# Kernel tuning notes

Measured on AMD Instinct MI355X. Metric: run time of the kernel, lower is better.

The kernel has to match this reference:

```python
import jax, jax.numpy as jnp
import numpy as np

B = 4
T, Hh, Ww = 16, 32, 32
C = 256
HEADS = 8
WIN = 4
SHIFT = 2
MLP = 1024


def _rel_pos_index(w):
    coords = np.stack(np.meshgrid(np.arange(w), np.arange(w), np.arange(w), indexing='ij')).reshape(3, -1)
    rc = (coords[:, :, None] - coords[:, None, :]).transpose(1, 2, 0)
    rc[:, :, 0] += w - 1
    rc[:, :, 1] += w - 1
    rc[:, :, 2] += w - 1
    rc[:, :, 0] *= (2 * w - 1) * (2 * w - 1)
    rc[:, :, 1] *= 2 * w - 1
    return rc.sum(-1).astype(np.int32)  # (w^3, w^3)


def _attn_mask(t, h, w, win, shift):
    m = np.zeros((t, h, w))
    sl = (slice(0, -win), slice(-win, -shift), slice(-shift, None))
    cnt = 0
    for a in sl:
        for b in sl:
            for c in sl:
                m[a, b, c] = cnt
                cnt += 1
    m = m.reshape(t // win, win, h // win, win, w // win, win).transpose(0, 2, 4, 1, 3, 5).reshape(-1, win ** 3)
    am = m[:, None, :] - m[:, :, None]  # (nW, N, N)
    return np.where(am != 0, -100.0, 0.0).astype(np.float32)


def setup_inputs() -> dict:
    key = jax.random.key(0)
    ks = jax.random.split(key, 12)
    s_in = 1.0 / np.sqrt(C)
    s_mlp = 1.0 / np.sqrt(MLP)
    return {
        'x': jax.random.normal(ks[0], (B, T * Hh * Ww, C), jnp.float32),
        'norm1_g': jnp.ones((C,), jnp.float32),
        'norm1_b': jnp.zeros((C,), jnp.float32),
        'qkv_w': jax.random.normal(ks[1], (C, 3 * C), jnp.float32) * s_in,
        'qkv_b': jax.random.normal(ks[2], (3 * C,), jnp.float32) * 0.02,
        'proj_w': jax.random.normal(ks[3], (C, C), jnp.float32) * s_in,
        'proj_b': jax.random.normal(ks[4], (C,), jnp.float32) * 0.02,
        'rel_bias_table': jax.random.normal(ks[5], ((2 * WIN - 1) ** 3, HEADS), jnp.float32) * 0.02,
        'norm2_g': jnp.ones((C,), jnp.float32),
        'norm2_b': jnp.zeros((C,), jnp.float32),
        'mlp_w1': jax.random.normal(ks[6], (C, MLP), jnp.float32) * s_in,
        'mlp_b1': jax.random.normal(ks[7], (MLP,), jnp.float32) * 0.02,
        'mlp_w2': jax.random.normal(ks[8], (MLP, C), jnp.float32) * s_mlp,
        'mlp_b2': jax.random.normal(ks[9], (C,), jnp.float32) * 0.02,
        'rel_index': jnp.asarray(_rel_pos_index(WIN)),
        'attn_mask': jnp.asarray(_attn_mask(T, Hh, Ww, WIN, SHIFT)),
    }


def _ln(x, g, b, eps):
    mu = x.mean(-1, keepdims=True)
    var = ((x - mu) ** 2).mean(-1, keepdims=True)
    return (x - mu) * jax.lax.rsqrt(var + eps) * g + b


def reference(x, norm1_g, norm1_b, qkv_w, qkv_b, proj_w, proj_b, rel_bias_table,
              norm2_g, norm2_b, mlp_w1, mlp_b1, mlp_w2, mlp_b2, rel_index, attn_mask):
    w = WIN
    N = w ** 3
    hd = C // HEADS
    scale = hd ** -0.5

    h = _ln(x, norm1_g, norm1_b, 1e-5).reshape(B, T, Hh, Ww, C)
    h = jnp.roll(h, shift=(-SHIFT, -SHIFT, -SHIFT), axis=(1, 2, 3))
    # window partition -> (B*nW, N, C)
    h = h.reshape(B, T // w, w, Hh // w, w, Ww // w, w, C)
    h = h.transpose(0, 1, 3, 5, 2, 4, 6, 7).reshape(-1, N, C)

    qkv = (h @ qkv_w + qkv_b).reshape(-1, N, 3, HEADS, hd)
    qkv = qkv.transpose(2, 0, 3, 1, 4)  # (3, BW, heads, N, hd)
    q, k, v = qkv[0] * scale, qkv[1], qkv[2]
    attn = jnp.einsum('bhid,bhjd->bhij', q, k)

    bias = rel_bias_table[rel_index.reshape(-1)].reshape(N, N, HEADS).transpose(2, 0, 1)
    attn = attn + bias[None]

    nW = attn_mask.shape[0]
    attn = attn.reshape(-1, nW, HEADS, N, N) + attn_mask[None, :, None]
    attn = jax.nn.softmax(attn.reshape(-1, HEADS, N, N), axis=-1)

    o = jnp.einsum('bhij,bhjd->bhid', attn, v).transpose(0, 2, 1, 3).reshape(-1, N, C)
    o = o @ proj_w + proj_b
    # window reverse
    o = o.reshape(B, T // w, Hh // w, Ww // w, w, w, w, C)
    o = o.transpose(0, 1, 4, 2, 5, 3, 6, 7).reshape(B, T, Hh, Ww, C)
    o = jnp.roll(o, shift=(SHIFT, SHIFT, SHIFT), axis=(1, 2, 3)).reshape(B, T * Hh * Ww, C)

    x = x + o
    y = _ln(x, norm2_g, norm2_b, 1e-6)
    y = jax.nn.gelu(y @ mlp_w1 + mlp_b1, approximate=False) @ mlp_w2 + mlp_b2
    return x + y
```

## Files before the change

kernel.cpp:

```cpp
#include <hip/hip_runtime.h>
#include <cstdint>
#include <cstddef>

typedef float  f32x4_t  __attribute__((ext_vector_type(4)));
typedef __bf16 bf16x8_t __attribute__((ext_vector_type(8)));
typedef __bf16 bf16x4_t __attribute__((ext_vector_type(4)));

#define NTOK   65536
#define CCH    256

__device__ __forceinline__ float wred_sum(float v) {
#pragma unroll
  for (int off = 32; off > 0; off >>= 1) v += __shfl_xor(v, off, 64);
  return v;
}

__device__ __forceinline__ void gload16(void* lds, const void* g) {
  __builtin_amdgcn_global_load_lds(
      (const __attribute__((address_space(1))) uint32_t*)g,
      (__attribute__((address_space(3))) uint32_t*)lds, 16, 0, 0);
}

__device__ __forceinline__ int win_to_orig(int token) {
  int gid = token >> 6, n = token & 63;
  int bb = gid >> 8, rem = gid & 255;
  int t = (((rem >> 6) << 2) + (n >> 4) + 2) & 15;
  int h = ((((rem >> 3) & 7) << 2) + ((n >> 2) & 3) + 2) & 31;
  int w = (((rem & 7) << 2) + (n & 3) + 2) & 31;
  return ((bb * 16 + t) * 32 + h) * 32 + w;
}

__device__ __forceinline__ float gelu_f(float v) {
  float u = v * (0.7978845608028654f + 0.03567740814f * v * v);
  float t = 1.0f - 2.0f / (__expf(2.0f * u) + 1.0f);
  return 0.5f * v * (1.0f + t);
}

__global__ __launch_bounds__(256) void prep_weights(
    const float* __restrict__ qkv_w, const float* __restrict__ proj_w,
    const float* __restrict__ mlp_w1, const float* __restrict__ mlp_w2,
    __bf16* __restrict__ wt_qkv, __bf16* __restrict__ wt_proj,
    __bf16* __restrict__ wt_mlp1, __bf16* __restrict__ wt_mlp2) {
  int i = blockIdx.x * 256 + threadIdx.x;
  if (i < 196608) {
    int k = i / 768, n = i % 768;
    wt_qkv[n * 256 + k] = (__bf16)qkv_w[i];
  } else if (i < 262144) {
    int j = i - 196608;
    int k = j >> 8, n = j & 255;
    wt_proj[n * 256 + k] = (__bf16)proj_w[j];
  } else if (i < 524288) {
    int j = i - 262144;
    int k = j >> 10, n = j & 1023;
    wt_mlp1[n * 256 + k] = (__bf16)mlp_w1[j];
  } else {
    int j = i - 524288;
    int k = j >> 8, n = j & 255;
    wt_mlp2[n * 1024 + k] = (__bf16)mlp_w2[j];
  }
}

__global__ __launch_bounds__(256) void cm_prep(
    const float* __restrict__ table, const int* __restrict__ ridx,
    const float* __restrict__ mask, __bf16* __restrict__ cm) {
  int tid = blockIdx.x * 256 + threadIdx.x;
  int l = tid & 63;
  int t16 = (tid >> 6) & 15;
  int h = (tid >> 10) & 7;
  int w = tid >> 13;
  int it = t16 & 3, jt = t16 >> 2;
  int i = it * 16 + (l & 15);
  int jb = jt * 16 + ((l >> 4) << 2);
  const float* mrow = mask + (size_t)w * 4096 + i * 64;
  const int* rrow = ridx + i * 64;
  bf16x4_t o;
#pragma unroll
  for (int r = 0; r < 4; ++r) {
    int j = jb + r;
    o[r] = (__bf16)(table[rrow[j] * 8 + h] + mrow[j]);
  }
  *(bf16x4_t*)(cm + (size_t)tid * 4) = o;
}

__global__ __launch_bounds__(256) void ln_kernel(
    const float* __restrict__ xin, const float* __restrict__ g,
    const float* __restrict__ b, __bf16* __restrict__ out, float eps) {
  int token = blockIdx.x * 4 + (threadIdx.x >> 6);
  int lane = threadIdx.x & 63;
  size_t src = (size_t)win_to_orig(token);
  f32x4_t v = ((const f32x4_t*)(xin + src * CCH))[lane];
  float mu = wred_sum(v[0] + v[1] + v[2] + v[3]) * (1.0f / 256.0f);
  float d0 = v[0] - mu, d1 = v[1] - mu, d2 = v[2] - mu, d3 = v[3] - mu;
  float var = wred_sum(d0 * d0 + d1 * d1 + d2 * d2 + d3 * d3) * (1.0f / 256.0f);
  float rs = rsqrtf(var + eps);
  f32x4_t gg = ((const f32x4_t*)g)[lane];
  f32x4_t bb = ((const f32x4_t*)b)[lane];
  bf16x4_t o;
  o[0] = (__bf16)(d0 * rs * gg[0] + bb[0]);
  o[1] = (__bf16)(d1 * rs * gg[1] + bb[1]);
  o[2] = (__bf16)(d2 * rs * gg[2] + bb[2]);
  o[3] = (__bf16)(d3 * rs * gg[3] + bb[3]);
  *(bf16x4_t*)(out + (size_t)token * CCH + lane * 4) = o;
}


#define GEMM_KLOOP(KT)                                                        \
  stage(0, 0);                                                                \
  asm volatile("s_waitcnt vmcnt(0)" ::: "memory");                            \
  __syncthreads();                                                            \
  _Pragma("unroll") for (int kt = 0; kt < (KT); ++kt) {                       \
    const int cur = kt & 1;                                                   \
    if (kt + 1 < (KT)) stage(cur ^ 1, kt + 1);                                \
    const __bf16* lA = smA[cur];                                              \
    const __bf16* lB = smB[cur];                                              \
    bf16x8_t af[4], wf[4];                                                    \
    _Pragma("unroll") for (int mm = 0; mm < 4; ++mm)                          \
        af[mm] = *(const bf16x8_t*)((const char*)lA + (mm * 16 + i15) * 64 +  \
                                    (((g ^ (i15 & 3))) << 4));                \
    _Pragma("unroll") for (int nn = 0; nn < 4; ++nn)                          \
        wf[nn] = *(const bf16x8_t*)((const char*)lB +                         \
                                    (wv * 64 + nn * 16 + i15) * 64 +          \
                                    (((g ^ (i15 & 3))) << 4));                \
    _Pragma("unroll") for (int nn = 0; nn < 4; ++nn)                          \
        _Pragma("unroll") for (int mm = 0; mm < 4; ++mm)                      \
            acc[nn][mm] = __builtin_amdgcn_mfma_f32_16x16x32_bf16(            \
                wf[nn], af[mm], acc[nn][mm], 0, 0, 0);                        \
    if (kt + 1 < (KT)) {                                                      \
      asm volatile("s_waitcnt vmcnt(0) lgkmcnt(0)" ::: "memory");             \
      __syncthreads();                                                        \
    }                                                                         \
  }

template <int N, int K, int EPI>
__global__ __launch_bounds__(256, 4) void gemm_c(
    const __bf16* __restrict__ A, const __bf16* __restrict__ Bt,
    const float* __restrict__ bias, const float* __restrict__ res,
    void* __restrict__ outp) {
  constexpr int KT = K / 32;
  constexpr int NX = N / 256;
  __shared__ __bf16 smA[2][64 * 32];
  __shared__ __bf16 smB[2][256 * 32];
  const int tid = threadIdx.x;
  const int wv = tid >> 6, ln = tid & 63;
  const int i15 = ln & 15, g = ln >> 4;

  int nwg = gridDim.x;
  int wgid = ((int)blockIdx.x & 7) * (nwg >> 3) + ((int)blockIdx.x >> 3);
  const int bx = wgid % NX, by = wgid / NX;
  const int bm = by * 64, bn = bx * 256;

  const int rowA = tid >> 2, chA = (tid & 3) ^ ((tid >> 2) & 3);
  const __bf16* aP = A + (size_t)(bm + rowA) * K + chA * 8;
  const __bf16* bP[4];
#pragma unroll
  for (int rnd = 0; rnd < 4; ++rnd) {
    int slot = rnd * 256 + tid;
    int row = slot >> 2, ch = (slot & 3) ^ (row & 3);
    bP[rnd] = Bt + (size_t)(bn + row) * K + ch * 8;
  }

  auto stage = [&](int buf, int kt) {
    gload16(&smA[buf][wv * 512], aP + kt * 32);
#pragma unroll
    for (int rnd = 0; rnd < 4; ++rnd)
      gload16(&smB[buf][rnd * 2048 + wv * 512], bP[rnd] + kt * 32);
  };

  f32x4_t acc[4][4];
#pragma unroll
  for (int nn = 0; nn < 4; ++nn)
#pragma unroll
    for (int mm = 0; mm < 4; ++mm) acc[nn][mm] = (f32x4_t){0.f, 0.f, 0.f, 0.f};

  GEMM_KLOOP(KT)

#pragma unroll
  for (int nn = 0; nn < 4; ++nn) {
    int colg = bn + wv * 64 + nn * 16 + g * 4;
    f32x4_t bv = *(const f32x4_t*)(bias + colg);
#pragma unroll
    for (int mm = 0; mm < 4; ++mm) {
      int rowg = bm + mm * 16 + i15;
      if constexpr (EPI == 0) {
        bf16x4_t o;
#pragma unroll
        for (int r = 0; r < 4; ++r) o[r] = (__bf16)(acc[nn][mm][r] + bv[r]);
        *(bf16x4_t*)((__bf16*)outp + (size_t)rowg * N + colg) = o;
      } else if constexpr (EPI == 1) {
        bf16x4_t o;
#pragma unroll
        for (int r = 0; r < 4; ++r)
          o[r] = (__bf16)gelu_f(acc[nn][mm][r] + bv[r]);
        *(bf16x4_t*)((__bf16*)outp + (size_t)rowg * N + colg) = o;
      } else {
        size_t off = (size_t)rowg * N + colg;
        f32x4_t rv = *(const f32x4_t*)(res + off);
        f32x4_t o;
#pragma unroll
        for (int r = 0; r < 4; ++r) o[r] = rv[r] + acc[nn][mm][r] + bv[r];
        *(f32x4_t*)((float*)outp + off) = o;
      }
    }
  }
}

__global__ __launch_bounds__(256, 4) void proj_ln(
    const __bf16* __restrict__ A, const __bf16* __restrict__ Bt,
    const float* __restrict__ bias, const float* __restrict__ res,
    const float* __restrict__ g2, const float* __restrict__ b2,
    float* __restrict__ x2, __bf16* __restrict__ yb) {
  constexpr int K = 256, KT = 8;
  __shared__ __bf16 smA[2][64 * 32];
  __shared__ __bf16 smB[2][256 * 32];
  __shared__ float2 stf[256];
  const int tid = threadIdx.x;
  const int wv = tid >> 6, ln = tid & 63;
  const int i15 = ln & 15, g = ln >> 4;

  int nwg = gridDim.x;
  int wgid = ((int)blockIdx.x & 7) * (nwg >> 3) + ((int)blockIdx.x >> 3);
  const int bm = wgid * 64;

  const int rowA = tid >> 2, chA = (tid & 3) ^ ((tid >> 2) & 3);
  const __bf16* aP = A + (size_t)(bm + rowA) * K + chA * 8;
  const __bf16* bP[4];
#pragma unroll
  for (int rnd = 0; rnd < 4; ++rnd) {
    int slot = rnd * 256 + tid;
    int row = slot >> 2, ch = (slot & 3) ^ (row & 3);
    bP[rnd] = Bt + (size_t)row * K + ch * 8;
  }

  auto stage = [&](int buf, int kt) {
    gload16(&smA[buf][wv * 512], aP + kt * 32);
#pragma unroll
    for (int rnd = 0; rnd < 4; ++rnd)
      gload16(&smB[buf][rnd * 2048 + wv * 512], bP[rnd] + kt * 32);
  };

  f32x4_t acc[4][4];
#pragma unroll
  for (int nn = 0; nn < 4; ++nn)
#pragma unroll
    for (int mm = 0; mm < 4; ++mm) acc[nn][mm] = (f32x4_t){0.f, 0.f, 0.f, 0.f};

  GEMM_KLOOP(KT)

  size_t dst[4];
#pragma unroll
  for (int mm = 0; mm < 4; ++mm)
    dst[mm] = (size_t)win_to_orig(bm + mm * 16 + i15) * CCH;
#pragma unroll
  for (int nn = 0; nn < 4; ++nn) {
    int colg = wv * 64 + nn * 16 + g * 4;
    f32x4_t bv = *(const f32x4_t*)(bias + colg);
#pragma unroll
    for (int mm = 0; mm < 4; ++mm) {
      f32x4_t rv = *(const f32x4_t*)(res + dst[mm] + colg);
#pragma unroll
      for (int r = 0; r < 4; ++r) acc[nn][mm][r] += bv[r] + rv[r];
    }
  }

#pragma unroll
  for (int mm = 0; mm < 4; ++mm) {
    float s1 = 0.f, s2 = 0.f;
#pragma unroll
    for (int nn = 0; nn < 4; ++nn)
#pragma unroll
      for (int r = 0; r < 4; ++r) {
        float v = acc[nn][mm][r];
        s1 += v;
        s2 += v * v;
      }
    s1 += __shfl_xor(s1, 16, 64);
    s1 += __shfl_xor(s1, 32, 64);
    s2 += __shfl_xor(s2, 16, 64);
    s2 += __shfl_xor(s2, 32, 64);
    if (g == 0) stf[(mm * 16 + i15) * 4 + wv] = make_float2(s1, s2);
  }
  __syncthreads();
  float mu[4], rs[4];
#pragma unroll
  for (int mm = 0; mm < 4; ++mm) {
    int row = mm * 16 + i15;
    float S1 = 0.f, S2 = 0.f;
#pragma unroll
    for (int w = 0; w < 4; ++w) {
      float2 p = stf[row * 4 + w];
      S1 += p.x;
      S2 += p.y;
    }
    mu[mm] = S1 * (1.0f / 256.0f);
    rs[mm] = rsqrtf(S2 * (1.0f / 256.0f) - mu[mm] * mu[mm] + 1e-6f);
  }

#pragma unroll
  for (int nn = 0; nn < 4; ++nn) {
    int colg = wv * 64 + nn * 16 + g * 4;
    f32x4_t gv = *(const f32x4_t*)(g2 + colg);
    f32x4_t bv = *(const f32x4_t*)(b2 + colg);
#pragma unroll
    for (int mm = 0; mm < 4; ++mm) {
      f32x4_t v = acc[nn][mm];
      *(f32x4_t*)(x2 + dst[mm] + colg) = v;
      bf16x4_t yo;
#pragma unroll
      for (int r = 0; r < 4; ++r)
        yo[r] = (__bf16)((v[r] - mu[mm]) * rs[mm] * gv[r] + bv[r]);
      *(bf16x4_t*)(yb + dst[mm] + colg) = yo;
    }
  }
}

__global__ __launch_bounds__(256) void attn_mfma(
    const __bf16* __restrict__ qkv, const __bf16* __restrict__ cm,
    __bf16* __restrict__ owin) {
  __shared__ __align__(16) __bf16 smP[4][64 * 72];
  __shared__ __align__(16) __bf16 smV[4][64 * 32];
  const int wv = threadIdx.x >> 6;
  const int ln = threadIdx.x & 63;
  const int task = blockIdx.x * 4 + wv;
  const int win = task >> 3;
  const int h = task & 7;
  const int i15 = ln & 15, g = ln >> 4;

  const __bf16* base = qkv + (size_t)win * 64 * 768 + h * 32;

  {
    __bf16* vdst = smV[wv];
#pragma unroll
    for (int c = 0; c < 4; ++c) {
      const __bf16* src =
          base + (size_t)(c * 16 + (ln >> 2)) * 768 + 512 + (ln & 3) * 8;
      gload16(vdst + c * 512, src);
    }
  }

  bf16x8_t kf[4], qf[4];
#pragma unroll
  for (int t = 0; t < 4; ++t) {
    kf[t] = *(const bf16x8_t*)(base + (size_t)(t * 16 + i15) * 768 + 256 + g * 8);
    qf[t] = *(const bf16x8_t*)(base + (size_t)(t * 16 + i15) * 768 + g * 8);
  }

  f32x4_t st[4][4];
#pragma unroll
  for (int jt = 0; jt < 4; ++jt)
#pragma unroll
    for (int it = 0; it < 4; ++it)
      st[jt][it] = __builtin_amdgcn_mfma_f32_16x16x32_bf16(
          kf[jt], qf[it], (f32x4_t){0.f, 0.f, 0.f, 0.f}, 0, 0, 0);

  const __bf16* cmp = cm + (((size_t)(win & 255) * 8 + h) * 16) * 256;
#pragma unroll
  for (int jt = 0; jt < 4; ++jt)
#pragma unroll
    for (int it = 0; it < 4; ++it) {
      bf16x4_t c4 = *(const bf16x4_t*)(cmp + ((jt * 4 + it) * 64 + ln) * 4);
#pragma unroll
      for (int r = 0; r < 4; ++r)
        st[jt][it][r] =
            fmaf(st[jt][it][r], 0.17677669529663687f, (float)c4[r]);
    }

#pragma unroll
  for (int it = 0; it < 4; ++it) {
    float mx = -1e30f;
#pragma unroll
    for (int jt = 0; jt < 4; ++jt)
#pragma unroll
      for (int r = 0; r < 4; ++r) mx = fmaxf(mx, st[jt][it][r]);
    mx = fmaxf(mx, __shfl_xor(mx, 16, 64));
    mx = fmaxf(mx, __shfl_xor(mx, 32, 64));
    float sum = 0.f;
#pragma unroll
    for (int jt = 0; jt < 4; ++jt)
#pragma unroll
      for (int r = 0; r < 4; ++r) {
        float p = __expf(st[jt][it][r] - mx);
        st[jt][it][r] = p;
        sum += p;
      }
    sum += __shfl_xor(sum, 16, 64);
    sum += __shfl_xor(sum, 32, 64);
    float inv = 1.0f / sum;
#pragma unroll
    for (int jt = 0; jt < 4; ++jt) {
      bf16x4_t p4;
#pragma unroll
      for (int r = 0; r < 4; ++r) p4[r] = (__bf16)(st[jt][it][r] * inv);
      *(bf16x4_t*)(smP[wv] + (it * 16 + i15) * 72 + jt * 16 + g * 4) = p4;
    }
  }
  __syncthreads();

  f32x4_t oacc[4][2];
#pragma unroll
  for (int it = 0; it < 4; ++it)
#pragma unroll
    for (int dt = 0; dt < 2; ++dt) oacc[it][dt] = (f32x4_t){0.f, 0.f, 0.f, 0.f};

  const __bf16* pl = smP[wv];
  const __bf16* vl = smV[wv];
#pragma unroll
  for (int kt = 0; kt < 2; ++kt) {
    bf16x8_t vf[2];
#pragma unroll
    for (int dt = 0; dt < 2; ++dt)
#pragma unroll
      for (int e = 0; e < 8; ++e)
        vf[dt][e] = vl[(kt * 32 + g * 8 + e) * 32 + dt * 16 + i15];
#pragma unroll
    for (int it = 0; it < 4; ++it) {
      bf16x8_t pa =
          *(const bf16x8_t*)(pl + (it * 16 + i15) * 72 + kt * 32 + g * 8);
#pragma unroll
      for (int dt = 0; dt < 2; ++dt)
        oacc[it][dt] = __builtin_amdgcn_mfma_f32_16x16x32_bf16(
            pa, vf[dt], oacc[it][dt], 0, 0, 0);
    }
  }

  __bf16* op = owin + (size_t)win * 64 * 256 + h * 32;
#pragma unroll
  for (int it = 0; it < 4; ++it)
#pragma unroll
    for (int r = 0; r < 4; ++r) {
      int i = it * 16 + g * 4 + r;
#pragma unroll
      for (int dt = 0; dt < 2; ++dt)
        op[(size_t)i * 256 + dt * 16 + i15] = (__bf16)oacc[it][dt][r];
    }
}

extern "C" void kernel_launch(void* const* d_in, const int* in_sizes, int n_in,
                              void* d_out, int out_size, void* d_ws,
                              size_t ws_size, hipStream_t stream) {
  (void)in_sizes; (void)n_in; (void)out_size; (void)ws_size;
  const float* x      = (const float*)d_in[0];
  const float* n1g    = (const float*)d_in[1];
  const float* n1b    = (const float*)d_in[2];
  const float* qkv_w  = (const float*)d_in[3];
  const float* qkv_b  = (const float*)d_in[4];
  const float* proj_w = (const float*)d_in[5];
  const float* proj_b = (const float*)d_in[6];
  const float* rbt    = (const float*)d_in[7];
  const float* n2g    = (const float*)d_in[8];
  const float* n2b    = (const float*)d_in[9];
  const float* mlp_w1 = (const float*)d_in[10];
  const float* mlp_b1 = (const float*)d_in[11];
  const float* mlp_w2 = (const float*)d_in[12];
  const float* mlp_b2 = (const float*)d_in[13];
  const int*   ridx   = (const int*)d_in[14];
  const float* amask  = (const float*)d_in[15];

  char* ws = (char*)d_ws;
  size_t off = 0;
  auto alloc = [&](size_t bytes) {
    void* p = ws + off;
    off += (bytes + 255) & ~(size_t)255;
    return p;
  };
  __bf16* wt_qkv  = (__bf16*)alloc(768 * 256 * 2);
  __bf16* wt_proj = (__bf16*)alloc(256 * 256 * 2);
  __bf16* wt_mlp1 = (__bf16*)alloc(1024 * 256 * 2);
  __bf16* wt_mlp2 = (__bf16*)alloc(1024 * 256 * 2);
  __bf16* hwin = (__bf16*)alloc((size_t)NTOK * 256 * 2);
  __bf16* qkv  = (__bf16*)alloc((size_t)NTOK * 768 * 2);
  __bf16* owin = (__bf16*)alloc((size_t)NTOK * 256 * 2);
  __bf16* cmb  = hwin;
  __bf16* yb   = hwin;
  __bf16* h1   = qkv;
  float* x2    = (float*)d_out;

  prep_weights<<<3072, 256, 0, stream>>>(qkv_w, proj_w, mlp_w1, mlp_w2,
                                         wt_qkv, wt_proj, wt_mlp1, wt_mlp2);
  ln_kernel<<<NTOK / 4, 256, 0, stream>>>(x, n1g, n1b, hwin, 1e-5f);
  gemm_c<768, 256, 0><<<3 * (NTOK / 64), 256, 0, stream>>>(
      hwin, wt_qkv, qkv_b, nullptr, qkv);
  cm_prep<<<8192, 256, 0, stream>>>(rbt, ridx, amask, cmb);
  attn_mfma<<<2048, 256, 0, stream>>>(qkv, cmb, owin);
  proj_ln<<<NTOK / 64, 256, 0, stream>>>(owin, wt_proj, proj_b, x, n2g, n2b,
                                         x2, yb);
  gemm_c<1024, 256, 1><<<4 * (NTOK / 64), 256, 0, stream>>>(
      yb, wt_mlp1, mlp_b1, nullptr, h1);
  gemm_c<256, 1024, 2><<<NTOK / 64, 256, 0, stream>>>(
      h1, wt_mlp2, mlp_b2, x2, d_out);
}
```

Baseline: 350.7 us.

## Enlarge GEMM tiles to 128x256x64 with 8 waves, single-buffered LDS

All four GEMM kernels (QKV, proj+LN, MLP1, MLP2) now use 128x256 output tiles with a K-step of 64 and 512-thread blocks arranged as a 2x4 wave grid, replacing 64x256 tiles with K-step 32 and 4 waves. The LDS swizzle widens to 8 chunks per row. The double-buffered prefetch pipeline is dropped in favour of a single buffer loaded, waited on and then consumed each iteration. The aim is more weight reuse per tile and fewer barriers per unit of K. The cost is that global loads no longer overlap with MFMA work, and LDS use per block grows to 48KB, which may lower occupancy.

```diff
diff --git a/kernel.cpp b/kernel.cpp
--- a/kernel.cpp
+++ b/kernel.cpp
@@ -103,84 +103,86 @@
   *(bf16x4_t*)(out + (size_t)token * CCH + lane * 4) = o;
 }
 
-
-#define GEMM_KLOOP(KT)                                                        \
-  stage(0, 0);                                                                \
-  asm volatile("s_waitcnt vmcnt(0)" ::: "memory");                            \
-  __syncthreads();                                                            \
-  _Pragma("unroll") for (int kt = 0; kt < (KT); ++kt) {                       \
-    const int cur = kt & 1;                                                   \
-    if (kt + 1 < (KT)) stage(cur ^ 1, kt + 1);                                \
-    const __bf16* lA = smA[cur];                                              \
-    const __bf16* lB = smB[cur];                                              \
-    bf16x8_t af[4], wf[4];                                                    \
-    _Pragma("unroll") for (int mm = 0; mm < 4; ++mm)                          \
-        af[mm] = *(const bf16x8_t*)((const char*)lA + (mm * 16 + i15) * 64 +  \
-                                    (((g ^ (i15 & 3))) << 4));                \
-    _Pragma("unroll") for (int nn = 0; nn < 4; ++nn)                          \
-        wf[nn] = *(const bf16x8_t*)((const char*)lB +                         \
-                                    (wv * 64 + nn * 16 + i15) * 64 +          \
-                                    (((g ^ (i15 & 3))) << 4));                \
-    _Pragma("unroll") for (int nn = 0; nn < 4; ++nn)                          \
-        _Pragma("unroll") for (int mm = 0; mm < 4; ++mm)                      \
-            acc[nn][mm] = __builtin_amdgcn_mfma_f32_16x16x32_bf16(            \
-                wf[nn], af[mm], acc[nn][mm], 0, 0, 0);                        \
-    if (kt + 1 < (KT)) {                                                      \
-      asm volatile("s_waitcnt vmcnt(0) lgkmcnt(0)" ::: "memory");             \
-      __syncthreads();                                                        \
-    }                                                                         \
+#define BMG 128
+#define BNG 256
+#define BKG 64
+
+#define GEMM_BODY(KT)                                                          \
+  f32x4_t acc[4][4];                                                           \
+  _Pragma("unroll") for (int nn = 0; nn < 4; ++nn)                             \
+      _Pragma("unroll") for (int mm = 0; mm < 4; ++mm)                         \
+          acc[nn][mm] = (f32x4_t){0.f, 0.f, 0.f, 0.f};                         \
+  for (int kt = 0; kt < (KT); ++kt) {                                          \
+    _Pragma("unroll") for (int it = 0; it < 2; ++it) {                         \
+      gload16(&smA[(it * 8 + wv) * 512], aP[it]);                              \
+      aP[it] += BKG;                                                           \
+    }                                                                          \
+    _Pragma("unroll") for (int it = 0; it < 4; ++it) {                         \
+      gload16(&smB[(it * 8 + wv) * 512], bP[it]);                              \
+      bP[it] += BKG;                                                           \
+    }                                                                          \
+    asm volatile("s_waitcnt vmcnt(0)" ::: "memory");                           \
+    __syncthreads();                                                           \
+    _Pragma("unroll") for (int kh = 0; kh < 2; ++kh) {                         \
+      int co = ((kh * 4 + g) ^ (i15 & 7)) * 16;                                \
+      bf16x8_t af[4], wf[4];                                                   \
+      _Pragma("unroll") for (int mm = 0; mm < 4; ++mm)                         \
+          af[mm] = *(const bf16x8_t*)((const char*)smA +                       \
+                                      (wr * 64 + mm * 16 + i15) * 128 + co);   \
+      _Pragma("unroll") for (int nn = 0; nn < 4; ++nn)                         \
+          wf[nn] = *(const bf16x8_t*)((const char*)smB +                       \
+                                      (wc * 64 + nn * 16 + i15) * 128 + co);   \
+      _Pragma("unroll") for (int nn = 0; nn < 4; ++nn)                         \
+          _Pragma("unroll") for (int mm = 0; mm < 4; ++mm)                     \
+              acc[nn][mm] = __builtin_amdgcn_mfma_f32_16x16x32_bf16(           \
+                  wf[nn], af[mm], acc[nn][mm], 0, 0, 0);                       \
+    }                                                                          \
+    __syncthreads();                                                           \
+  }
+
+#define GEMM_SETUP(Abase, Bbase, K)                                            \
+  const __bf16* aP[2];                                                         \
+  const __bf16* bP[4];                                                         \
+  _Pragma("unroll") for (int it = 0; it < 2; ++it) {                           \
+    int slot = (it * 8 + wv) * 64 + ln;                                        \
+    int row = slot >> 3, chunk = (slot & 7) ^ (row & 7);                       \
+    aP[it] = (Abase) + (size_t)(bm + row) * (K) + chunk * 8;                   \
+  }                                                                            \
+  _Pragma("unroll") for (int it = 0; it < 4; ++it) {                           \
+    int slot = (it * 8 + wv) * 64 + ln;                                        \
+    int row = slot >> 3, chunk = (slot & 7) ^ (row & 7);                       \
+    bP[it] = (Bbase) + (size_t)(bn + row) * (K) + chunk * 8;                   \
   }
 
 template <int N, int K, int EPI>
-__global__ __launch_bounds__(256, 4) void gemm_c(
+__global__ __launch_bounds__(512, 4) void gemm_kernel(
     const __bf16* __restrict__ A, const __bf16* __restrict__ Bt,
     const float* __restrict__ bias, const float* __restrict__ res,
     void* __restrict__ outp) {
-  constexpr int KT = K / 32;
-  constexpr int NX = N / 256;
-  __shared__ __bf16 smA[2][64 * 32];
-  __shared__ __bf16 smB[2][256 * 32];
-  const int tid = threadIdx.x;
-  const int wv = tid >> 6, ln = tid & 63;
+  constexpr int KT = K / BKG;
+  constexpr int NX = N / BNG;
+  __shared__ __bf16 smA[BMG * BKG];
+  __shared__ __bf16 smB[BNG * BKG];
+  const int wv = threadIdx.x >> 6;
+  const int ln = threadIdx.x & 63;
   const int i15 = ln & 15, g = ln >> 4;
 
   int nwg = gridDim.x;
   int wgid = ((int)blockIdx.x & 7) * (nwg >> 3) + ((int)blockIdx.x >> 3);
   const int bx = wgid % NX, by = wgid / NX;
-  const int bm = by * 64, bn = bx * 256;
-
-  const int rowA = tid >> 2, chA = (tid & 3) ^ ((tid >> 2) & 3);
-  const __bf16* aP = A + (size_t)(bm + rowA) * K + chA * 8;
-  const __bf16* bP[4];
-#pragma unroll
-  for (int rnd = 0; rnd < 4; ++rnd) {
-    int slot = rnd * 256 + tid;
-    int row = slot >> 2, ch = (slot & 3) ^ (row & 3);
-    bP[rnd] = Bt + (size_t)(bn + row) * K + ch * 8;
-  }
-
-  auto stage = [&](int buf, int kt) {
-    gload16(&smA[buf][wv * 512], aP + kt * 32);
-#pragma unroll
-    for (int rnd = 0; rnd < 4; ++rnd)
-      gload16(&smB[buf][rnd * 2048 + wv * 512], bP[rnd] + kt * 32);
-  };
-
-  f32x4_t acc[4][4];
-#pragma unroll
-  for (int nn = 0; nn < 4; ++nn)
-#pragma unroll
-    for (int mm = 0; mm < 4; ++mm) acc[nn][mm] = (f32x4_t){0.f, 0.f, 0.f, 0.f};
-
-  GEMM_KLOOP(KT)
+  const int bm = by * BMG, bn = bx * BNG;
+  const int wr = wv >> 2, wc = wv & 3;
+
+  GEMM_SETUP(A, Bt, K)
+  GEMM_BODY(KT)
 
 #pragma unroll
   for (int nn = 0; nn < 4; ++nn) {
-    int colg = bn + wv * 64 + nn * 16 + g * 4;
+    int colg = bn + wc * 64 + nn * 16 + g * 4;
     f32x4_t bv = *(const f32x4_t*)(bias + colg);
 #pragma unroll
     for (int mm = 0; mm < 4; ++mm) {
-      int rowg = bm + mm * 16 + i15;
+      int rowg = bm + wr * 64 + mm * 16 + i15;
       if constexpr (EPI == 0) {
         bf16x4_t o;
 #pragma unroll
@@ -204,55 +206,34 @@
   }
 }
 
-__global__ __launch_bounds__(256, 4) void proj_ln(
+__global__ __launch_bounds__(512, 4) void proj_ln(
     const __bf16* __restrict__ A, const __bf16* __restrict__ Bt,
     const float* __restrict__ bias, const float* __restrict__ res,
     const float* __restrict__ g2, const float* __restrict__ b2,
     float* __restrict__ x2, __bf16* __restrict__ yb) {
-  constexpr int K = 256, KT = 8;
-  __shared__ __bf16 smA[2][64 * 32];
-  __shared__ __bf16 smB[2][256 * 32];
-  __shared__ float2 stf[256];
-  const int tid = threadIdx.x;
-  const int wv = tid >> 6, ln = tid & 63;
+  constexpr int K = 256, KT = 4;
+  __shared__ __bf16 smA[BMG * BKG];
+  __shared__ __bf16 smB[BNG * BKG];
+  __shared__ float2 stf[512];
+  const int wv = threadIdx.x >> 6;
+  const int ln = threadIdx.x & 63;
   const int i15 = ln & 15, g = ln >> 4;
 
   int nwg = gridDim.x;
   int wgid = ((int)blockIdx.x & 7) * (nwg >> 3) + ((int)blockIdx.x >> 3);
-  const int bm = wgid * 64;
-
-  const int rowA = tid >> 2, chA = (tid & 3) ^ ((tid >> 2) & 3);
-  const __bf16* aP = A + (size_t)(bm + rowA) * K + chA * 8;
-  const __bf16* bP[4];
-#pragma unroll
-  for (int rnd = 0; rnd < 4; ++rnd) {
-    int slot = rnd * 256 + tid;
-    int row = slot >> 2, ch = (slot & 3) ^ (row & 3);
-    bP[rnd] = Bt + (size_t)row * K + ch * 8;
-  }
-
-  auto stage = [&](int buf, int kt) {
-    gload16(&smA[buf][wv * 512], aP + kt * 32);
-#pragma unroll
-    for (int rnd = 0; rnd < 4; ++rnd)
-      gload16(&smB[buf][rnd * 2048 + wv * 512], bP[rnd] + kt * 32);
-  };
-
-  f32x4_t acc[4][4];
-#pragma unroll
-  for (int nn = 0; nn < 4; ++nn)
-#pragma unroll
-    for (int mm = 0; mm < 4; ++mm) acc[nn][mm] = (f32x4_t){0.f, 0.f, 0.f, 0.f};
-
-  GEMM_KLOOP(KT)
+  const int bm = wgid * BMG, bn = 0;
+  const int wr = wv >> 2, wc = wv & 3;
+
+  GEMM_SETUP(A, Bt, K)
+  GEMM_BODY(KT)
 
   size_t dst[4];
 #pragma unroll
   for (int mm = 0; mm < 4; ++mm)
-    dst[mm] = (size_t)win_to_orig(bm + mm * 16 + i15) * CCH;
+    dst[mm] = (size_t)win_to_orig(bm + wr * 64 + mm * 16 + i15) * CCH;
 #pragma unroll
   for (int nn = 0; nn < 4; ++nn) {
-    int colg = wv * 64 + nn * 16 + g * 4;
+    int colg = wc * 64 + nn * 16 + g * 4;
     f32x4_t bv = *(const f32x4_t*)(bias + colg);
 #pragma unroll
     for (int mm = 0; mm < 4; ++mm) {
@@ -277,13 +258,13 @@
     s1 += __shfl_xor(s1, 32, 64);
     s2 += __shfl_xor(s2, 16, 64);
     s2 += __shfl_xor(s2, 32, 64);
-    if (g == 0) stf[(mm * 16 + i15) * 4 + wv] = make_float2(s1, s2);
+    if (g == 0) stf[(wr * 64 + mm * 16 + i15) * 4 + wc] = make_float2(s1, s2);
   }
   __syncthreads();
   float mu[4], rs[4];
 #pragma unroll
   for (int mm = 0; mm < 4; ++mm) {
-    int row = mm * 16 + i15;
+    int row = wr * 64 + mm * 16 + i15;
     float S1 = 0.f, S2 = 0.f;
 #pragma unroll
     for (int w = 0; w < 4; ++w) {
@@ -297,7 +278,7 @@
 
 #pragma unroll
   for (int nn = 0; nn < 4; ++nn) {
-    int colg = wv * 64 + nn * 16 + g * 4;
+    int colg = wc * 64 + nn * 16 + g * 4;
     f32x4_t gv = *(const f32x4_t*)(g2 + colg);
     f32x4_t bv = *(const f32x4_t*)(b2 + colg);
 #pragma unroll
@@ -477,14 +458,14 @@
   prep_weights<<<3072, 256, 0, stream>>>(qkv_w, proj_w, mlp_w1, mlp_w2,
                                          wt_qkv, wt_proj, wt_mlp1, wt_mlp2);
   ln_kernel<<<NTOK / 4, 256, 0, stream>>>(x, n1g, n1b, hwin, 1e-5f);
-  gemm_c<768, 256, 0><<<3 * (NTOK / 64), 256, 0, stream>>>(
+  gemm_kernel<768, 256, 0><<<3 * (NTOK / BMG), 512, 0, stream>>>(
       hwin, wt_qkv, qkv_b, nullptr, qkv);
   cm_prep<<<8192, 256, 0, stream>>>(rbt, ridx, amask, cmb);
   attn_mfma<<<2048, 256, 0, stream>>>(qkv, cmb, owin);
-  proj_ln<<<NTOK / 64, 256, 0, stream>>>(owin, wt_proj, proj_b, x, n2g, n2b,
-                                         x2, yb);
-  gemm_c<1024, 256, 1><<<4 * (NTOK / 64), 256, 0, stream>>>(
+  proj_ln<<<NTOK / BMG, 512, 0, stream>>>(owin, wt_proj, proj_b, x, n2g, n2b,
+                                          x2, yb);
+  gemm_kernel<1024, 256, 1><<<4 * (NTOK / BMG), 512, 0, stream>>>(
       yb, wt_mlp1, mlp_b1, nullptr, h1);
-  gemm_c<256, 1024, 2><<<NTOK / 64, 256, 0, stream>>>(
+  gemm_kernel<256, 1024, 2><<<NTOK / BMG, 512, 0, stream>>>(
       h1, wt_mlp2, mlp_b2, x2, d_out);
 }
```

New measurement: 382.2 us. +9.0%, slower.
